# Kernel tuning notes

Measured on AMD Instinct MI355X. Metric: run time of the kernel, lower is better.

The kernel has to match this reference:

```python
import jax, jax.numpy as jnp
import numpy as np

DIM = 512          # model dim
DH = 32            # dim_head
WSZ = 8            # window_size
HEADS = DIM // DH  # 16
INNER = HEADS * DH # 512
D4 = DIM // 4      # DPB hidden = 128
EPS = 1e-5


def _ln(x, g, b=None, eps=EPS):
    m = jnp.mean(x, axis=-1, keepdims=True)
    v = jnp.var(x, axis=-1, keepdims=True)
    y = (x - m) * jax.lax.rsqrt(v + eps) * g
    return y if b is None else y + b


def setup_inputs() -> dict:
    key = jax.random.key(0)
    ks = jax.random.split(key, 8)
    g = lambda k, shape, s=0.02: (jax.random.normal(k, shape, jnp.float32) * s)
    return {
        "x": jax.random.normal(ks[0], (16, 64, 64, DIM), jnp.float32),
        "norm_g": jnp.ones((DIM,), jnp.float32),
        "norm_b": jnp.zeros((DIM,), jnp.float32),
        "w_qkv": g(ks[1], (DIM, 3 * INNER)),
        "w_out": g(ks[2], (INNER, DIM)),
        "b_out": jnp.zeros((DIM,), jnp.float32),
        "dpb_w0": g(ks[3], (2, D4)), "dpb_b0": jnp.zeros((D4,), jnp.float32), "dpb_ln0": jnp.ones((D4,), jnp.float32),
        "dpb_w1": g(ks[4], (D4, D4)), "dpb_b1": jnp.zeros((D4,), jnp.float32), "dpb_ln1": jnp.ones((D4,), jnp.float32),
        "dpb_w2": g(ks[5], (D4, D4)), "dpb_b2": jnp.zeros((D4,), jnp.float32), "dpb_ln2": jnp.ones((D4,), jnp.float32),
        "dpb_w3": g(ks[6], (D4, 1)), "dpb_b3": jnp.zeros((1,), jnp.float32),
    }


def reference(x, norm_g, norm_b, w_qkv, w_out, b_out,
              dpb_w0, dpb_b0, dpb_ln0,
              dpb_w1, dpb_b1, dpb_ln1,
              dpb_w2, dpb_b2, dpb_ln2,
              dpb_w3, dpb_b3):
    B, H, W, d = x.shape
    w = WSZ
    scale = DH ** -0.5

    x = _ln(x, norm_g, norm_b)

    # 'short' attention: partition into non-overlapping wxw windows
    # b (h s1) (w s2) d -> (b h w) s1 s2 d
    xw = x.reshape(B, H // w, w, W // w, w, d).transpose(0, 1, 3, 2, 4, 5)
    xw = xw.reshape(-1, w, w, d)  # [nb, w, w, d]

    qkv = xw @ w_qkv  # 1x1 conv == dense, no bias
    q, k, v = jnp.split(qkv, 3, axis=-1)
    to_heads = lambda t: t.reshape(t.shape[0], w * w, HEADS, DH).transpose(0, 2, 1, 3)
    q, k, v = map(to_heads, (q, k, v))  # [nb, h, w*w, dh]

    sim = jnp.einsum('bhid,bhjd->bhij', q * scale, k)  # [nb, h, w*w, w*w]

    # relative-position gather indices (static)
    pos = jnp.arange(w)
    grid = jnp.stack(jnp.meshgrid(pos, pos, indexing='ij'), axis=-1).reshape(-1, 2)
    rel = grid[:, None] - grid[None, :] + (w - 1)
    rel_pos_indices = rel[..., 0] * (2 * w - 1) + rel[..., 1]  # [w*w, w*w]

    # dynamic position bias MLP over the (2w+1)^2 relative offsets
    p = jnp.arange(-w, w + 1)
    rp = jnp.stack(jnp.meshgrid(p, p, indexing='ij'), axis=-1).reshape(-1, 2).astype(jnp.float32)
    h = jax.nn.relu(_ln(rp @ dpb_w0 + dpb_b0, dpb_ln0))
    h = jax.nn.relu(_ln(h @ dpb_w1 + dpb_b1, dpb_ln1))
    h = jax.nn.relu(_ln(h @ dpb_w2 + dpb_b2, dpb_ln2))
    biases = (h @ dpb_w3 + dpb_b3)[:, 0]  # [(2w+1)^2]

    sim = sim + biases[rel_pos_indices]
    attn = jax.nn.softmax(sim, axis=-1)
    out = jnp.einsum('bhij,bhjd->bhid', attn, v)

    out = out.transpose(0, 2, 1, 3).reshape(-1, w, w, INNER)
    out = out @ w_out + b_out  # 1x1 conv with bias

    # (b h w) s1 s2 d -> b (h s1) (w s2) d
    out = out.reshape(B, H // w, W // w, w, w, d).transpose(0, 1, 3, 2, 4, 5)
    return out.reshape(B, H, W, d)
```

## Files before the change

### kernel.cpp

```cpp
#include <hip/hip_runtime.h>
#include <cstdint>
#include <cstddef>

typedef unsigned short u16;
typedef __attribute__((ext_vector_type(8))) short short8;
typedef __attribute__((ext_vector_type(4))) float f32x4;
typedef __attribute__((ext_vector_type(4))) unsigned short us4;

#define AS1 __attribute__((address_space(1)))
#define AS3 __attribute__((address_space(3)))

__device__ __forceinline__ u16 f2bf(float f) {
  union { float f; unsigned u; } v; v.f = f;
  unsigned r = v.u + 0x7fffu + ((v.u >> 16) & 1u);
  return (u16)(r >> 16);
}

__device__ __forceinline__ void gload_lds16(const u16* g, u16* l) {
  __builtin_amdgcn_global_load_lds((AS1 void*)g, (AS3 void*)l, 16, 0, 0);
}

__global__ void ln_cast_kernel(const float* __restrict__ x, const float* __restrict__ g,
                               const float* __restrict__ b, u16* __restrict__ out) {
  const int lane = threadIdx.x & 63;
  const int tok = blockIdx.x * 4 + (threadIdx.x >> 6);
  const float4* row = (const float4*)(x + (size_t)tok * 512);
  float4 v0 = row[lane];
  float4 v1 = row[lane + 64];
  float s = v0.x + v0.y + v0.z + v0.w + v1.x + v1.y + v1.z + v1.w;
  float q = v0.x*v0.x + v0.y*v0.y + v0.z*v0.z + v0.w*v0.w
          + v1.x*v1.x + v1.y*v1.y + v1.z*v1.z + v1.w*v1.w;
#pragma unroll
  for (int m = 1; m < 64; m <<= 1) { s += __shfl_xor(s, m, 64); q += __shfl_xor(q, m, 64); }
  const float mean = s * (1.0f / 512.0f);
  const float var = q * (1.0f / 512.0f) - mean * mean;
  const float r = rsqrtf(var + 1e-5f);
  const float4* g4 = (const float4*)g;
  const float4* b4 = (const float4*)b;
  float4 ga = g4[lane], gb = g4[lane + 64];
  float4 ba = b4[lane], bb = b4[lane + 64];
  us4 o0 = { f2bf((v0.x - mean) * r * ga.x + ba.x), f2bf((v0.y - mean) * r * ga.y + ba.y),
             f2bf((v0.z - mean) * r * ga.z + ba.z), f2bf((v0.w - mean) * r * ga.w + ba.w) };
  us4 o1 = { f2bf((v1.x - mean) * r * gb.x + bb.x), f2bf((v1.y - mean) * r * gb.y + bb.y),
             f2bf((v1.z - mean) * r * gb.z + bb.z), f2bf((v1.w - mean) * r * gb.w + bb.w) };
  *(us4*)(out + (size_t)tok * 512 + lane * 4) = o0;
  *(us4*)(out + (size_t)tok * 512 + 256 + lane * 4) = o1;
}

__global__ void prep_w_kernel(const float* __restrict__ wqkv, const float* __restrict__ wout,
                              u16* __restrict__ wqkvT, u16* __restrict__ woutT) {
  int idx = blockIdx.x * blockDim.x + threadIdx.x;
  if (idx < 512 * 1536) {
    int n = idx >> 9, k = idx & 511;
    wqkvT[idx] = f2bf(wqkv[k * 1536 + n]);
  } else {
    int j = idx - 512 * 1536;
    if (j < 512 * 512) {
      int n = j >> 9, k = j & 511;
      woutT[j] = f2bf(wout[k * 512 + n]);
    }
  }
}

__device__ __forceinline__ float lnrelu128(float a, float g, float* red, int tid) {
  float s = a, q = a * a;
#pragma unroll
  for (int m = 1; m < 64; m <<= 1) { s += __shfl_xor(s, m, 64); q += __shfl_xor(q, m, 64); }
  __syncthreads();
  if ((tid & 63) == 0) { red[tid >> 6] = s; red[2 + (tid >> 6)] = q; }
  __syncthreads();
  float S = red[0] + red[1], Q = red[2] + red[3];
  float mean = S * (1.f / 128.f);
  float var = Q * (1.f / 128.f) - mean * mean;
  float y = (a - mean) * rsqrtf(var + 1e-5f) * g;
  return fmaxf(y, 0.f);
}

__global__ void dpb_mlp_kernel(const float* __restrict__ w0, const float* __restrict__ b0, const float* __restrict__ g0,
                               const float* __restrict__ w1, const float* __restrict__ b1, const float* __restrict__ g1,
                               const float* __restrict__ w2, const float* __restrict__ b2, const float* __restrict__ g2,
                               const float* __restrict__ w3, const float* __restrict__ b3,
                               float* __restrict__ biases) {
  __shared__ float h[128];
  __shared__ float red[4];
  const int tid = threadIdx.x;
  const int row = blockIdx.x;
  const float p0 = (float)(row / 17) - 8.0f;
  const float p1 = (float)(row % 17) - 8.0f;
  float a = p0 * w0[tid] + p1 * w0[128 + tid] + b0[tid];
  a = lnrelu128(a, g0[tid], red, tid);
  h[tid] = a;
  __syncthreads();
  float acc = b1[tid];
  for (int i = 0; i < 128; ++i) acc += h[i] * w1[i * 128 + tid];
  acc = lnrelu128(acc, g1[tid], red, tid);
  h[tid] = acc;
  __syncthreads();
  float acc2 = b2[tid];
  for (int i = 0; i < 128; ++i) acc2 += h[i] * w2[i * 128 + tid];
  acc2 = lnrelu128(acc2, g2[tid], red, tid);
  float t = acc2 * w3[tid];
#pragma unroll
  for (int m = 1; m < 64; m <<= 1) t += __shfl_xor(t, m, 64);
  __syncthreads();
  if ((tid & 63) == 0) red[tid >> 6] = t;
  __syncthreads();
  if (tid == 0) biases[row] = red[0] + red[1] + b3[0];
}

__global__ void dpb_table_kernel(const float* __restrict__ biases, float* __restrict__ table) {
  int t = blockIdx.x * blockDim.x + threadIdx.x;
  if (t < 4096) {
    int i = t >> 6, j = t & 63;
    int r0 = (i >> 3) - (j >> 3) + 7;
    int r1 = (i & 7) - (j & 7) + 7;
    table[t] = biases[r0 * 15 + r1];
  }
}

template <int N, bool F32OUT>
__global__ __launch_bounds__(256) void gemm_bt_kernel(const u16* __restrict__ A, const u16* __restrict__ BT,
                                                      void* __restrict__ Cv, const float* __restrict__ bias) {
  __shared__ __align__(16) u16 As[128 * 32];
  __shared__ __align__(16) u16 Bs[128 * 32];
  const int tid = threadIdx.x;
  const int w = tid >> 6, l = tid & 63;
  const int wr = w >> 1, wc = w & 1;
  const int cr = l & 15, cg = l >> 4;
  const size_t brow = (size_t)blockIdx.x * 128;
  const int bcol = blockIdx.y * 128;

  const f32x4 zero = {0.f, 0.f, 0.f, 0.f};
  f32x4 acc[4][4];
#pragma unroll
  for (int i = 0; i < 4; ++i)
#pragma unroll
    for (int j = 0; j < 4; ++j) acc[i][j] = zero;

  const int srow = l >> 2;
  const int scol = ((l & 3) ^ (srow & 3)) * 8;
  const u16* gA0 = A + (brow + (size_t)w * 32 + srow) * 512 + scol;
  const u16* gB0 = BT + ((size_t)bcol + w * 32 + srow) * 512 + scol;
  u16* lA0 = &As[w * 1024];
  u16* lA1 = &As[w * 1024 + 512];
  u16* lB0 = &Bs[w * 1024];
  u16* lB1 = &Bs[w * 1024 + 512];

  for (int k0 = 0; k0 < 512; k0 += 32) {
    gload_lds16(gA0 + k0, lA0);
    gload_lds16(gA0 + k0 + 16 * 512, lA1);
    gload_lds16(gB0 + k0, lB0);
    gload_lds16(gB0 + k0 + 16 * 512, lB1);
    __syncthreads();
    short8 af[4], bf[4];
#pragma unroll
    for (int mt = 0; mt < 4; ++mt) {
      int r = wr * 64 + mt * 16 + cr;
      af[mt] = *(const short8*)&As[r * 32 + ((cg ^ (r & 3)) * 8)];
    }
#pragma unroll
    for (int nt = 0; nt < 4; ++nt) {
      int r = wc * 64 + nt * 16 + cr;
      bf[nt] = *(const short8*)&Bs[r * 32 + ((cg ^ (r & 3)) * 8)];
    }
#pragma unroll
    for (int mt = 0; mt < 4; ++mt)
#pragma unroll
      for (int nt = 0; nt < 4; ++nt)
        acc[mt][nt] = __builtin_amdgcn_mfma_f32_16x16x32_bf16(af[mt], bf[nt], acc[mt][nt], 0, 0, 0);
    __syncthreads();
  }

  if (F32OUT) {
    float* C = (float*)Cv;
#pragma unroll
    for (int nt = 0; nt < 4; ++nt) {
      int col = bcol + wc * 64 + nt * 16 + cr;
      float bv = bias[col];
#pragma unroll
      for (int mt = 0; mt < 4; ++mt)
#pragma unroll
        for (int reg = 0; reg < 4; ++reg) {
          size_t r = brow + wr * 64 + mt * 16 + cg * 4 + reg;
          C[r * N + col] = acc[mt][nt][reg] + bv;
        }
    }
  } else {
    u16* C = (u16*)Cv;
#pragma unroll
    for (int nt = 0; nt < 4; ++nt) {
      int col = bcol + wc * 64 + nt * 16 + cr;
#pragma unroll
      for (int mt = 0; mt < 4; ++mt)
#pragma unroll
        for (int reg = 0; reg < 4; ++reg) {
          size_t r = brow + wr * 64 + mt * 16 + cg * 4 + reg;
          C[r * N + col] = f2bf(acc[mt][nt][reg]);
        }
    }
  }
}

__global__ __launch_bounds__(64) void attn_kernel(const u16* __restrict__ qkv,
                                                  const float* __restrict__ table,
                                                  u16* __restrict__ aout) {
  __shared__ __align__(16) u16 P[64 * 72];
  __shared__ __align__(16) u16 VT[32 * 72];
  const int l = threadIdx.x;
  const int cr = l & 15, cg = l >> 4;
  const int head = blockIdx.x & 15;
  const int win = blockIdx.x >> 4;
  const int base = ((win >> 6) << 12) + (((win >> 3) & 7) << 9) + ((win & 7) << 3);

  {
    const size_t row = base + ((l >> 3) << 6) + (l & 7);
    const u16* vp = qkv + row * 1536 + 1024 + head * 32;
    short8 v0 = *(const short8*)(vp);
    short8 v1 = *(const short8*)(vp + 8);
    short8 v2 = *(const short8*)(vp + 16);
    short8 v3 = *(const short8*)(vp + 24);
#pragma unroll
    for (int j = 0; j < 8; ++j) {
      VT[j * 72 + l] = (u16)v0[j];
      VT[(8 + j) * 72 + l] = (u16)v1[j];
      VT[(16 + j) * 72 + l] = (u16)v2[j];
      VT[(24 + j) * 72 + l] = (u16)v3[j];
    }
  }

  short8 qf[4], kf[4];
#pragma unroll
  for (int mt = 0; mt < 4; ++mt) {
    int t = mt * 16 + cr;
    size_t row = base + ((t >> 3) << 6) + (t & 7);
    qf[mt] = *(const short8*)(qkv + row * 1536 + head * 32 + cg * 8);
    kf[mt] = *(const short8*)(qkv + row * 1536 + 512 + head * 32 + cg * 8);
  }

  const f32x4 zero = {0.f, 0.f, 0.f, 0.f};
  f32x4 s[4][4];
#pragma unroll
  for (int mt = 0; mt < 4; ++mt)
#pragma unroll
    for (int nt = 0; nt < 4; ++nt)
      s[mt][nt] = __builtin_amdgcn_mfma_f32_16x16x32_bf16(qf[mt], kf[nt], zero, 0, 0, 0);

  const float scale = 0.17677669529663689f;
#pragma unroll
  for (int mt = 0; mt < 4; ++mt) {
#pragma unroll
    for (int reg = 0; reg < 4; ++reg) {
      const int r = mt * 16 + cg * 4 + reg;
      float v[4];
      float mx = -3.0e38f;
#pragma unroll
      for (int nt = 0; nt < 4; ++nt) {
        v[nt] = s[mt][nt][reg] * scale + table[r * 64 + nt * 16 + cr];
        mx = fmaxf(mx, v[nt]);
      }
#pragma unroll
      for (int m2 = 1; m2 < 16; m2 <<= 1) mx = fmaxf(mx, __shfl_xor(mx, m2, 64));
      float sum = 0.f;
#pragma unroll
      for (int nt = 0; nt < 4; ++nt) { v[nt] = __expf(v[nt] - mx); sum += v[nt]; }
#pragma unroll
      for (int m2 = 1; m2 < 16; m2 <<= 1) sum += __shfl_xor(sum, m2, 64);
      float inv = 1.0f / sum;
#pragma unroll
      for (int nt = 0; nt < 4; ++nt) P[r * 72 + nt * 16 + cr] = f2bf(v[nt] * inv);
    }
  }
  __syncthreads();

  f32x4 o[4][2];
#pragma unroll
  for (int mt = 0; mt < 4; ++mt) { o[mt][0] = zero; o[mt][1] = zero; }
#pragma unroll
  for (int kk = 0; kk < 2; ++kk) {
    short8 pf[4], vf[2];
#pragma unroll
    for (int mt = 0; mt < 4; ++mt) pf[mt] = *(const short8*)&P[(mt * 16 + cr) * 72 + kk * 32 + cg * 8];
#pragma unroll
    for (int n2 = 0; n2 < 2; ++n2) vf[n2] = *(const short8*)&VT[(n2 * 16 + cr) * 72 + kk * 32 + cg * 8];
#pragma unroll
    for (int mt = 0; mt < 4; ++mt)
#pragma unroll
      for (int n2 = 0; n2 < 2; ++n2)
        o[mt][n2] = __builtin_amdgcn_mfma_f32_16x16x32_bf16(pf[mt], vf[n2], o[mt][n2], 0, 0, 0);
  }

#pragma unroll
  for (int mt = 0; mt < 4; ++mt)
#pragma unroll
    for (int n2 = 0; n2 < 2; ++n2)
#pragma unroll
      for (int reg = 0; reg < 4; ++reg) {
        int t = mt * 16 + cg * 4 + reg;
        size_t row = base + ((t >> 3) << 6) + (t & 7);
        aout[row * 512 + head * 32 + n2 * 16 + cr] = f2bf(o[mt][n2][reg]);
      }
}

extern "C" void kernel_launch(void* const* d_in, const int* in_sizes, int n_in,
                              void* d_out, int out_size, void* d_ws, size_t ws_size,
                              hipStream_t stream) {
  const float* x = (const float*)d_in[0];
  const float* norm_g = (const float*)d_in[1];
  const float* norm_b = (const float*)d_in[2];
  const float* w_qkv = (const float*)d_in[3];
  const float* w_out = (const float*)d_in[4];
  const float* b_out = (const float*)d_in[5];
  const float* dw0 = (const float*)d_in[6];
  const float* db0 = (const float*)d_in[7];
  const float* dg0 = (const float*)d_in[8];
  const float* dw1 = (const float*)d_in[9];
  const float* db1 = (const float*)d_in[10];
  const float* dg1 = (const float*)d_in[11];
  const float* dw2 = (const float*)d_in[12];
  const float* db2 = (const float*)d_in[13];
  const float* dg2 = (const float*)d_in[14];
  const float* dw3 = (const float*)d_in[15];
  const float* db3 = (const float*)d_in[16];

  char* ws = (char*)d_ws;
  u16* xln = (u16*)(ws);
  u16* wqkvT = (u16*)(ws + 67108864);
  u16* woutT = (u16*)(ws + 68681728);
  float* biases = (float*)(ws + 69206016);
  float* table = (float*)(ws + 69210112);
  u16* qkvbuf = (u16*)(ws + 69226496);
  u16* attnbuf = (u16*)(ws + 119558144);

  ln_cast_kernel<<<16384, 256, 0, stream>>>(x, norm_g, norm_b, xln);
  prep_w_kernel<<<4096, 256, 0, stream>>>(w_qkv, w_out, wqkvT, woutT);
  dpb_mlp_kernel<<<289, 128, 0, stream>>>(dw0, db0, dg0, dw1, db1, dg1, dw2, db2, dg2, dw3, db3, biases);
  dpb_table_kernel<<<16, 256, 0, stream>>>(biases, table);

  for (int c = 0; c < 4; ++c) {
    const u16* Ac = xln + (size_t)c * 16384 * 512;
    gemm_bt_kernel<1536, false><<<dim3(128, 12), 256, 0, stream>>>(Ac, wqkvT, (void*)qkvbuf, nullptr);
    attn_kernel<<<4096, 64, 0, stream>>>(qkvbuf, table, attnbuf);
    float* Cc = (float*)d_out + (size_t)c * 16384 * 512;
    gemm_bt_kernel<512, true><<<dim3(128, 4), 256, 0, stream>>>(attnbuf, woutT, (void*)Cc, b_out);
  }
}
```

Baseline: 414.6 us.

## Replace GEMM with 256x256-tile double-buffered pipelined kernel and adaptive chunking

Replaces the 128x128 single-buffered bf16 GEMM with a 256x256-tile, 512-thread kernel. It double-buffers LDS loads with global_load_lds and interleaves staging and MFMA phases under barriers and setprio. Blocks are remapped with an XCD-aware index swizzle, and the number of row chunks is now picked from the workspace size, so fewer launches run when memory allows. This targets low MFMA utilisation and load latency in the GEMMs, at the cost of 128KB LDS per block, heavy register pressure, and fewer blocks for small chunks.

```diff
diff --git a/kernel.cpp b/kernel.cpp
--- a/kernel.cpp
+++ b/kernel.cpp
@@ -118,84 +118,158 @@
   }
 }
 
-template <int N, bool F32OUT>
-__global__ __launch_bounds__(256) void gemm_bt_kernel(const u16* __restrict__ A, const u16* __restrict__ BT,
-                                                      void* __restrict__ Cv, const float* __restrict__ bias) {
-  __shared__ __align__(16) u16 As[128 * 32];
-  __shared__ __align__(16) u16 Bs[128 * 32];
+template <int CT, bool F32OUT>
+__global__ __launch_bounds__(512, 2) void gemm256_kernel(const u16* __restrict__ A, const u16* __restrict__ BT,
+                                                         void* __restrict__ Cv, const float* __restrict__ bias) {
+  __shared__ __align__(16) u16 lds[65536];
   const int tid = threadIdx.x;
   const int w = tid >> 6, l = tid & 63;
-  const int wr = w >> 1, wc = w & 1;
+  const int wm = w >> 2, wn = w & 3;
   const int cr = l & 15, cg = l >> 4;
-  const size_t brow = (size_t)blockIdx.x * 128;
-  const int bcol = blockIdx.y * 128;
+  const int pc8 = (cg ^ ((cr + (cr >> 2)) & 3)) * 8;
+
+  const int nwg = gridDim.x;
+  const int q = nwg >> 3;
+  const int swz = (blockIdx.x & 7) * q + (blockIdx.x >> 3);
+  const int rt = swz / CT, ct = swz % CT;
+  const size_t brow = (size_t)rt * 256;
+  const size_t bcol = (size_t)ct * 256;
+  const int N = CT * 256;
+
+  const int srow = tid >> 2;
+  const int sch8 = ((tid & 3) ^ ((srow + (srow >> 2)) & 3)) * 8;
 
   const f32x4 zero = {0.f, 0.f, 0.f, 0.f};
-  f32x4 acc[4][4];
-#pragma unroll
-  for (int i = 0; i < 4; ++i)
+  f32x4 acc[8][4];
+#pragma unroll
+  for (int i = 0; i < 8; ++i)
 #pragma unroll
     for (int j = 0; j < 4; ++j) acc[i][j] = zero;
 
-  const int srow = l >> 2;
-  const int scol = ((l & 3) ^ (srow & 3)) * 8;
-  const u16* gA0 = A + (brow + (size_t)w * 32 + srow) * 512 + scol;
-  const u16* gB0 = BT + ((size_t)bcol + w * 32 + srow) * 512 + scol;
-  u16* lA0 = &As[w * 1024];
-  u16* lA1 = &As[w * 1024 + 512];
-  u16* lB0 = &Bs[w * 1024];
-  u16* lB1 = &Bs[w * 1024 + 512];
-
-  for (int k0 = 0; k0 < 512; k0 += 32) {
-    gload_lds16(gA0 + k0, lA0);
-    gload_lds16(gA0 + k0 + 16 * 512, lA1);
-    gload_lds16(gB0 + k0, lB0);
-    gload_lds16(gB0 + k0 + 16 * 512, lB1);
-    __syncthreads();
-    short8 af[4], bf[4];
-#pragma unroll
-    for (int mt = 0; mt < 4; ++mt) {
-      int r = wr * 64 + mt * 16 + cr;
-      af[mt] = *(const short8*)&As[r * 32 + ((cg ^ (r & 3)) * 8)];
-    }
-#pragma unroll
-    for (int nt = 0; nt < 4; ++nt) {
-      int r = wc * 64 + nt * 16 + cr;
-      bf[nt] = *(const short8*)&Bs[r * 32 + ((cg ^ (r & 3)) * 8)];
-    }
-#pragma unroll
-    for (int mt = 0; mt < 4; ++mt)
-#pragma unroll
-      for (int nt = 0; nt < 4; ++nt)
-        acc[mt][nt] = __builtin_amdgcn_mfma_f32_16x16x32_bf16(af[mt], bf[nt], acc[mt][nt], 0, 0, 0);
-    __syncthreads();
-  }
+  const u16* aP = &lds[(wm * 128 + cr) * 32 + pc8];
+  const u16* bP = &lds[(wn * 64 + cr) * 32 + pc8];
+
+#define STAGE_HALF(G, GROW0, KCOL, LBASE)                                          \
+  do {                                                                             \
+    const u16* g0_ = (G) + ((GROW0) + srow) * 512 + (KCOL) + sch8;                 \
+    gload_lds16(g0_, &lds[(LBASE) + w * 512]);                                     \
+    gload_lds16(g0_ + 128 * 512, &lds[(LBASE) + 4096 + w * 512]);                  \
+  } while (0)
+
+  STAGE_HALF(A, brow, 0, 0);
+  STAGE_HALF(BT, bcol, 0, 32768);
+  STAGE_HALF(A, brow, 32, 8192);
+  STAGE_HALF(BT, bcol, 32, 32768 + 8192);
+  asm volatile("s_waitcnt vmcnt(4)" ::: "memory");
+  __builtin_amdgcn_s_barrier();
+  __builtin_amdgcn_sched_barrier(0);
+
+#pragma unroll 2
+  for (int kt = 0; kt < 8; ++kt) {
+    const int cur = kt & 1;
+    const int nbuf = cur ^ 1;
+    const int ktn = (kt < 7) ? kt + 1 : 7;
+    const int kcn = ktn * 64;
+    const int abase = cur * 16384;
+    const int bbase = 32768 + cur * 16384;
+    short8 af[8], bfr[2];
+
+#pragma unroll
+    for (int fr = 0; fr < 8; ++fr) af[fr] = *(const short8*)(aP + abase + fr * 512);
+#pragma unroll
+    for (int c = 0; c < 2; ++c) bfr[c] = *(const short8*)(bP + bbase + c * 512);
+    STAGE_HALF(A, brow, kcn, nbuf * 16384);
+    __builtin_amdgcn_s_barrier();
+    __builtin_amdgcn_sched_barrier(0);
+    __builtin_amdgcn_s_setprio(1);
+#pragma unroll
+    for (int fr = 0; fr < 8; ++fr) {
+      acc[fr][0] = __builtin_amdgcn_mfma_f32_16x16x32_bf16(af[fr], bfr[0], acc[fr][0], 0, 0, 0);
+      acc[fr][1] = __builtin_amdgcn_mfma_f32_16x16x32_bf16(af[fr], bfr[1], acc[fr][1], 0, 0, 0);
+    }
+    __builtin_amdgcn_s_setprio(0);
+    __builtin_amdgcn_s_barrier();
+    __builtin_amdgcn_sched_barrier(0);
+
+#pragma unroll
+    for (int c = 0; c < 2; ++c) bfr[c] = *(const short8*)(bP + bbase + (2 + c) * 512);
+    STAGE_HALF(BT, bcol, kcn, 32768 + nbuf * 16384);
+    __builtin_amdgcn_s_barrier();
+    __builtin_amdgcn_sched_barrier(0);
+    __builtin_amdgcn_s_setprio(1);
+#pragma unroll
+    for (int fr = 0; fr < 8; ++fr) {
+      acc[fr][2] = __builtin_amdgcn_mfma_f32_16x16x32_bf16(af[fr], bfr[0], acc[fr][2], 0, 0, 0);
+      acc[fr][3] = __builtin_amdgcn_mfma_f32_16x16x32_bf16(af[fr], bfr[1], acc[fr][3], 0, 0, 0);
+    }
+    __builtin_amdgcn_s_setprio(0);
+    asm volatile("s_waitcnt vmcnt(4)" ::: "memory");
+    __builtin_amdgcn_s_barrier();
+    __builtin_amdgcn_sched_barrier(0);
+
+#pragma unroll
+    for (int fr = 0; fr < 8; ++fr) af[fr] = *(const short8*)(aP + abase + 8192 + fr * 512);
+#pragma unroll
+    for (int c = 0; c < 2; ++c) bfr[c] = *(const short8*)(bP + bbase + 8192 + c * 512);
+    STAGE_HALF(A, brow, kcn + 32, nbuf * 16384 + 8192);
+    __builtin_amdgcn_s_barrier();
+    __builtin_amdgcn_sched_barrier(0);
+    __builtin_amdgcn_s_setprio(1);
+#pragma unroll
+    for (int fr = 0; fr < 8; ++fr) {
+      acc[fr][0] = __builtin_amdgcn_mfma_f32_16x16x32_bf16(af[fr], bfr[0], acc[fr][0], 0, 0, 0);
+      acc[fr][1] = __builtin_amdgcn_mfma_f32_16x16x32_bf16(af[fr], bfr[1], acc[fr][1], 0, 0, 0);
+    }
+    __builtin_amdgcn_s_setprio(0);
+    __builtin_amdgcn_s_barrier();
+    __builtin_amdgcn_sched_barrier(0);
+
+#pragma unroll
+    for (int c = 0; c < 2; ++c) bfr[c] = *(const short8*)(bP + bbase + 8192 + (2 + c) * 512);
+    STAGE_HALF(BT, bcol, kcn + 32, 32768 + nbuf * 16384 + 8192);
+    __builtin_amdgcn_s_barrier();
+    __builtin_amdgcn_sched_barrier(0);
+    __builtin_amdgcn_s_setprio(1);
+#pragma unroll
+    for (int fr = 0; fr < 8; ++fr) {
+      acc[fr][2] = __builtin_amdgcn_mfma_f32_16x16x32_bf16(af[fr], bfr[0], acc[fr][2], 0, 0, 0);
+      acc[fr][3] = __builtin_amdgcn_mfma_f32_16x16x32_bf16(af[fr], bfr[1], acc[fr][3], 0, 0, 0);
+    }
+    __builtin_amdgcn_s_setprio(0);
+    asm volatile("s_waitcnt vmcnt(4)" ::: "memory");
+    __builtin_amdgcn_s_barrier();
+    __builtin_amdgcn_sched_barrier(0);
+  }
+#undef STAGE_HALF
+
+  asm volatile("s_waitcnt vmcnt(0)" ::: "memory");
+  __builtin_amdgcn_sched_barrier(0);
 
   if (F32OUT) {
     float* C = (float*)Cv;
 #pragma unroll
-    for (int nt = 0; nt < 4; ++nt) {
-      int col = bcol + wc * 64 + nt * 16 + cr;
+    for (int fc = 0; fc < 4; ++fc) {
+      size_t col = bcol + wn * 64 + fc * 16 + cr;
       float bv = bias[col];
 #pragma unroll
-      for (int mt = 0; mt < 4; ++mt)
+      for (int fr = 0; fr < 8; ++fr)
 #pragma unroll
         for (int reg = 0; reg < 4; ++reg) {
-          size_t r = brow + wr * 64 + mt * 16 + cg * 4 + reg;
-          C[r * N + col] = acc[mt][nt][reg] + bv;
+          size_t r = brow + wm * 128 + fr * 16 + cg * 4 + reg;
+          C[r * N + col] = acc[fr][fc][reg] + bv;
         }
     }
   } else {
     u16* C = (u16*)Cv;
 #pragma unroll
-    for (int nt = 0; nt < 4; ++nt) {
-      int col = bcol + wc * 64 + nt * 16 + cr;
-#pragma unroll
-      for (int mt = 0; mt < 4; ++mt)
+    for (int fc = 0; fc < 4; ++fc) {
+      size_t col = bcol + wn * 64 + fc * 16 + cr;
+#pragma unroll
+      for (int fr = 0; fr < 8; ++fr)
 #pragma unroll
         for (int reg = 0; reg < 4; ++reg) {
-          size_t r = brow + wr * 64 + mt * 16 + cg * 4 + reg;
-          C[r * N + col] = f2bf(acc[mt][nt][reg]);
+          size_t r = brow + wm * 128 + fr * 16 + cg * 4 + reg;
+          C[r * N + col] = f2bf(acc[fr][fc][reg]);
         }
     }
   }
@@ -323,24 +397,32 @@
   const float* db3 = (const float*)d_in[16];
 
   char* ws = (char*)d_ws;
-  u16* xln = (u16*)(ws);
-  u16* wqkvT = (u16*)(ws + 67108864);
-  u16* woutT = (u16*)(ws + 68681728);
-  float* biases = (float*)(ws + 69206016);
-  float* table = (float*)(ws + 69210112);
-  u16* qkvbuf = (u16*)(ws + 69226496);
-  u16* attnbuf = (u16*)(ws + 119558144);
+  size_t off = 0;
+  auto take = [&](size_t bytes) { char* p = ws + off; off += (bytes + 255) & ~(size_t)255; return p; };
+  u16* xln = (u16*)take(65536ull * 512 * 2);
+  u16* wqkvT = (u16*)take(1536 * 512 * 2);
+  u16* woutT = (u16*)take(512 * 512 * 2);
+  float* biases = (float*)take(289 * 4);
+  float* table = (float*)take(4096 * 4);
+
+  size_t rem = (ws_size > off) ? ws_size - off : 0;
+  int nch = 4;
+  if (rem >= 65536ull * 2048 * 2 + 512) nch = 1;
+  else if (rem >= 32768ull * 2048 * 2 + 512) nch = 2;
+  const int rows = 65536 / nch;
+  u16* qkvbuf = (u16*)take((size_t)rows * 1536 * 2);
+  u16* attnbuf = (u16*)take((size_t)rows * 512 * 2);
 
   ln_cast_kernel<<<16384, 256, 0, stream>>>(x, norm_g, norm_b, xln);
   prep_w_kernel<<<4096, 256, 0, stream>>>(w_qkv, w_out, wqkvT, woutT);
   dpb_mlp_kernel<<<289, 128, 0, stream>>>(dw0, db0, dg0, dw1, db1, dg1, dw2, db2, dg2, dw3, db3, biases);
   dpb_table_kernel<<<16, 256, 0, stream>>>(biases, table);
 
-  for (int c = 0; c < 4; ++c) {
-    const u16* Ac = xln + (size_t)c * 16384 * 512;
-    gemm_bt_kernel<1536, false><<<dim3(128, 12), 256, 0, stream>>>(Ac, wqkvT, (void*)qkvbuf, nullptr);
-    attn_kernel<<<4096, 64, 0, stream>>>(qkvbuf, table, attnbuf);
-    float* Cc = (float*)d_out + (size_t)c * 16384 * 512;
-    gemm_bt_kernel<512, true><<<dim3(128, 4), 256, 0, stream>>>(attnbuf, woutT, (void*)Cc, b_out);
-  }
-}
+  for (int c = 0; c < nch; ++c) {
+    const u16* Ac = xln + (size_t)c * rows * 512;
+    gemm256_kernel<6, false><<<(rows / 256) * 6, 512, 0, stream>>>(Ac, wqkvT, (void*)qkvbuf, nullptr);
+    attn_kernel<<<(rows / 64) * 16, 64, 0, stream>>>(qkvbuf, table, attnbuf);
+    float* Cc = (float*)d_out + (size_t)c * rows * 512;
+    gemm256_kernel<2, true><<<(rows / 256) * 2, 512, 0, stream>>>(attnbuf, woutT, (void*)Cc, b_out);
+  }
+}
```

New measurement: 379.7 us. 1.09x faster.
